# Kernel optimization log

Hardware: AMD Instinct MI355X
Metric: run time of the kernel (lower is better)

Reference implementation:

```python
import jax, jax.numpy as jnp
import numpy as np

V = 50257   # vocab
P = 2048    # max positions
D = 768     # hidden
H = 12      # heads
F = 3072    # 4*D ffn
NL = 12     # layers
L = 2048    # seq len
EPS = 1e-5


def setup_inputs() -> dict:
    key = jax.random.key(0)
    ks = jax.random.split(key, 12)
    r = lambda k, shp: jax.random.normal(k, shp, jnp.float32) * 0.02
    return dict(
        input_ids=jax.random.randint(ks[0], (1, L), 0, V, dtype=jnp.int32),
        attention_mask=jnp.ones((1, L), jnp.int32),
        wte=r(ks[1], (V, D)),
        wpe=r(ks[2], (P, D)),
        lnf_w=jnp.ones((D,), jnp.float32),
        lnf_b=jnp.zeros((D,), jnp.float32),
        ln1_w=jnp.ones((NL, D), jnp.float32),
        ln1_b=jnp.zeros((NL, D), jnp.float32),
        qw=r(ks[3], (NL, D, D)),
        kw=r(ks[4], (NL, D, D)),
        vw=r(ks[5], (NL, D, D)),
        ow=r(ks[6], (NL, D, D)),
        ob=jnp.zeros((NL, D), jnp.float32),
        ln2_w=jnp.ones((NL, D), jnp.float32),
        ln2_b=jnp.zeros((NL, D), jnp.float32),
        fcw=r(ks[7], (NL, D, F)),
        fcb=jnp.zeros((NL, F), jnp.float32),
        pw=r(ks[8], (NL, F, D)),
        pb=jnp.zeros((NL, D), jnp.float32),
    )


def _ln(x, w, b):
    mu = jnp.mean(x, -1, keepdims=True)
    var = jnp.mean((x - mu) ** 2, -1, keepdims=True)
    return (x - mu) * jax.lax.rsqrt(var + EPS) * w + b


def reference(input_ids, attention_mask, wte, wpe, lnf_w, lnf_b,
              ln1_w, ln1_b, qw, kw, vw, ow, ob, ln2_w, ln2_b,
              fcw, fcb, pw, pb):
    ids = input_ids.reshape(-1, input_ids.shape[-1])          # [1, L]
    pos = jnp.cumsum(attention_mask, -1) - 1
    pos = jnp.where(attention_mask == 0, 1, pos)
    h = (wte[ids] + wpe[pos])[0]                               # [L, D]

    key_valid = attention_mask[0] > 0                          # actual_length mask
    mask = jnp.tril(jnp.ones((L, L), bool)) & key_valid[None, :]  # causal+pad
    dh = D // H

    def layer(h, p):
        l1w, l1b, Wq, Wk, Wv, Wo, bo, l2w, l2b, Wf, bf, Wp, bp = p
        x = _ln(h, l1w, l1b)
        q = (x @ Wq).reshape(L, H, dh)
        k = (x @ Wk).reshape(L, H, dh)
        v = (x @ Wv).reshape(L, H, dh)
        # GPT-Neo attention: NO 1/sqrt(dh) scaling
        scores = jnp.einsum('qhd,khd->hqk', q, k)
        scores = jnp.where(mask[None], scores, jnp.float32(-1e9))
        attn = jax.nn.softmax(scores, axis=-1)
        ctx = jnp.einsum('hqk,khd->qhd', attn, v).reshape(L, D)
        h = h + ctx @ Wo + bo
        y = _ln(h, l2w, l2b)
        h = h + jax.nn.gelu(y @ Wf + bf, approximate=True) @ Wp + bp
        return h, None

    h, _ = jax.lax.scan(layer, h, (ln1_w, ln1_b, qw, kw, vw, ow, ob,
                                   ln2_w, ln2_b, fcw, fcb, pw, pb))
    return _ln(h[None, :, :], lnf_w, lnf_b)                    # [1, L, D]
```

## Files before the change

kernel.cpp:

```cpp
#include <hip/hip_runtime.h>
#include <hip/hip_bf16.h>
#include <math.h>
#include <stdint.h>

#define L 2048
#define D 768
#define H 12
#define DH 64
#define F 3072
#define NL 12
#define QKVN 2304

typedef __attribute__((ext_vector_type(8))) short bf16x8;
typedef __attribute__((ext_vector_type(4))) float f32x4;

__device__ __forceinline__ ushort f2bf(float x) {
    union { float f; uint32_t u; } c; c.f = x;
    uint32_t r = c.u + 0x7FFFu + ((c.u >> 16) & 1u);
    return (ushort)(r >> 16);
}

__device__ __forceinline__ uint32_t cvt_pk_bf16(float lo, float hi) {
    uint32_t r;
    asm("v_cvt_pk_bf16_f32 %0, %1, %2" : "=v"(r) : "v"(lo), "v"(hi));
    return r;
}

__device__ __forceinline__ bf16x8 ldfrag(const ushort* p) {
    ushort4 lo = *(const ushort4*)(p);
    ushort4 hi = *(const ushort4*)(p + 16);
    bf16x8 f;
    f[0] = (short)lo.x; f[1] = (short)lo.y; f[2] = (short)lo.z; f[3] = (short)lo.w;
    f[4] = (short)hi.x; f[5] = (short)hi.y; f[6] = (short)hi.z; f[7] = (short)hi.w;
    return f;
}

__device__ __forceinline__ float gelu_tanh(float x) {
    float c = 0.7978845608028654f;
    float inner = c * (x + 0.044715f * x * x * x);
    return 0.5f * x * (1.0f + tanhf(inner));
}

__global__ void pos_kernel(const int* __restrict__ mask, int* __restrict__ pos) {
    __shared__ int sm[L];
    for (int i = threadIdx.x; i < L; i += blockDim.x) sm[i] = mask[i];
    __syncthreads();
    int t = blockIdx.x * blockDim.x + threadIdx.x;
    if (t < L) {
        int s = 0;
        for (int j = 0; j <= t; ++j) s += sm[j];
        int p = s - 1;
        if (sm[t] == 0) p = 1;
        pos[t] = p;
    }
}

__global__ void maskb_kernel(const int* __restrict__ mask, float* __restrict__ mb) {
    int i = blockIdx.x * blockDim.x + threadIdx.x;
    if (i < L) mb[i] = mask[i] ? 0.f : -1e9f;
}

__global__ __launch_bounds__(256) void embed_kernel(const int* __restrict__ ids,
                                                    const int* __restrict__ pos,
                                                    const float* __restrict__ wte,
                                                    const float* __restrict__ wpe,
                                                    float* __restrict__ h) {
    int t = blockIdx.x;
    int id = ids[t];
    int p = pos[t];
    const float* we = wte + (size_t)id * D;
    const float* wp = wpe + (size_t)p * D;
    float* hr = h + (size_t)t * D;
#pragma unroll
    for (int i = 0; i < 3; ++i) {
        int d = threadIdx.x + i * 256;
        hr[d] = we[d] + wp[d];
    }
}

template <bool OUTBF>
__global__ __launch_bounds__(256) void ln_kernel(const float* __restrict__ in,
                                                 const float* __restrict__ w,
                                                 const float* __restrict__ b,
                                                 float* __restrict__ outF,
                                                 ushort* __restrict__ outB) {
    __shared__ float red[2][4];
    int row = blockIdx.x;
    const float* x = in + (size_t)row * D;
    int t = threadIdx.x;
    float v0 = x[t], v1 = x[t + 256], v2 = x[t + 512];
    float s = v0 + v1 + v2;
    float ss = v0 * v0 + v1 * v1 + v2 * v2;
#pragma unroll
    for (int o = 32; o; o >>= 1) {
        s += __shfl_xor(s, o);
        ss += __shfl_xor(ss, o);
    }
    int wave = t >> 6;
    if ((t & 63) == 0) { red[0][wave] = s; red[1][wave] = ss; }
    __syncthreads();
    s = red[0][0] + red[0][1] + red[0][2] + red[0][3];
    ss = red[1][0] + red[1][1] + red[1][2] + red[1][3];
    float mean = s * (1.f / D);
    float var = ss * (1.f / D) - mean * mean;
    float rstd = rsqrtf(var + 1e-5f);
#pragma unroll
    for (int i = 0; i < 3; ++i) {
        int d = t + i * 256;
        float vv = (i == 0) ? v0 : (i == 1) ? v1 : v2;
        float y = (vv - mean) * rstd * w[d] + b[d];
        if (OUTBF) outB[(size_t)row * D + d] = f2bf(y);
        else       outF[(size_t)row * D + d] = y;
    }
}

__global__ __launch_bounds__(256) void tcast_f32(const float* __restrict__ in,
                                                 ushort* __restrict__ out,
                                                 int K, int N,
                                                 size_t inStride, size_t outStride) {
    in += blockIdx.z * inStride;
    out += blockIdx.z * outStride;
    __shared__ float tile[64][65];
    int k0 = blockIdx.y * 64, n0 = blockIdx.x * 64;
    int t = threadIdx.x;
    int cl = t & 63, rg = t >> 6;
#pragma unroll
    for (int i = 0; i < 16; ++i) {
        int r = rg + 4 * i;
        tile[r][cl] = in[(size_t)(k0 + r) * N + n0 + cl];
    }
    __syncthreads();
#pragma unroll
    for (int i = 0; i < 16; ++i) {
        int r = rg + 4 * i;
        out[(size_t)(n0 + r) * K + k0 + cl] = f2bf(tile[cl][r]);
    }
}

template <int ACT, bool OUTBF, bool VSPLIT>
__global__ __launch_bounds__(256) void gemm_bf16(const ushort* __restrict__ A,
                                                 const ushort* __restrict__ Bt,
                                                 const float* __restrict__ bias,
                                                 const float* __restrict__ resid,
                                                 float* __restrict__ outF,
                                                 ushort* __restrict__ outB,
                                                 ushort* __restrict__ vTout,
                                                 int M, int N, int K) {
    __shared__ __align__(16) char lds[32768];
    const int tid = threadIdx.x;
    const int lane = tid & 63, w = tid >> 6;
    const int wr = w >> 1, wc = w & 1;
    const int bm = blockIdx.y * 128, bn = blockIdx.x * 128;
    const int l15 = lane & 15, l4 = lane >> 4;
    const int srow = tid >> 2, c = tid & 3;
    const int blo = (c & 1) * 32 + (c >> 1) * 8;

    const int sxor = (srow & 3) << 4;
    const int wo0 = srow * 64 + (blo ^ sxor);
    const int wo1 = srow * 64 + ((blo + 16) ^ sxor);
    const int rxor = (l4 * 16) ^ ((l15 & 3) << 4);
    const int aBase = (wr * 64 + l15) * 64 + rxor;
    const int bBase = (wc * 64 + l15) * 64 + rxor;

    f32x4 acc[4][4];
#pragma unroll
    for (int m = 0; m < 4; ++m)
#pragma unroll
        for (int n = 0; n < 4; ++n)
            acc[m][n] = (f32x4){0.f, 0.f, 0.f, 0.f};

    const ushort* Ag = A + (size_t)(bm + srow) * K + c * 8;
    const ushort* Ag2 = Ag + (size_t)64 * K;
    const ushort* Bg = Bt + (size_t)(bn + srow) * K + c * 8;
    const ushort* Bg2 = Bg + (size_t)64 * K;

    uint4 a0 = *(const uint4*)(Ag);
    uint4 a1 = *(const uint4*)(Ag2);
    uint4 b0 = *(const uint4*)(Bg);
    uint4 b1 = *(const uint4*)(Bg2);

    for (int k0 = 0; k0 < K; k0 += 32) {
        char* Ab = lds + ((k0 >> 5) & 1) * 16384;
        char* Bb = Ab + 8192;
        uint2 t0, t1;
        t0.x = a0.x; t0.y = a0.y; t1.x = a0.z; t1.y = a0.w;
        *(uint2*)(Ab + wo0) = t0;
        *(uint2*)(Ab + wo1) = t1;
        t0.x = a1.x; t0.y = a1.y; t1.x = a1.z; t1.y = a1.w;
        *(uint2*)(Ab + wo0 + 4096) = t0;
        *(uint2*)(Ab + wo1 + 4096) = t1;
        t0.x = b0.x; t0.y = b0.y; t1.x = b0.z; t1.y = b0.w;
        *(uint2*)(Bb + wo0) = t0;
        *(uint2*)(Bb + wo1) = t1;
        t0.x = b1.x; t0.y = b1.y; t1.x = b1.z; t1.y = b1.w;
        *(uint2*)(Bb + wo0 + 4096) = t0;
        *(uint2*)(Bb + wo1 + 4096) = t1;
        __syncthreads();
        if (k0 + 32 < K) {
            a0 = *(const uint4*)(Ag + k0 + 32);
            a1 = *(const uint4*)(Ag2 + k0 + 32);
            b0 = *(const uint4*)(Bg + k0 + 32);
            b1 = *(const uint4*)(Bg2 + k0 + 32);
        }
        bf16x8 af[4], bfv[4];
#pragma unroll
        for (int m = 0; m < 4; ++m)
            af[m] = *(const bf16x8*)(Ab + aBase + m * 1024);
#pragma unroll
        for (int n = 0; n < 4; ++n)
            bfv[n] = *(const bf16x8*)(Bb + bBase + n * 1024);
#pragma unroll
        for (int m = 0; m < 4; ++m)
#pragma unroll
            for (int n = 0; n < 4; ++n)
                acc[m][n] = __builtin_amdgcn_mfma_f32_16x16x32_bf16(af[m], bfv[n], acc[m][n], 0, 0, 0);
    }

#pragma unroll
    for (int m = 0; m < 4; ++m)
#pragma unroll
        for (int n = 0; n < 4; ++n) {
            int col = bn + wc * 64 + n * 16 + l15;
            int row0 = bm + wr * 64 + m * 16 + l4 * 4;
            if (VSPLIT && col >= 2 * D) {
                ushort4 pk;
                pk.x = f2bf(acc[m][n][0]);
                pk.y = f2bf(acc[m][n][1]);
                pk.z = f2bf(acc[m][n][2]);
                pk.w = f2bf(acc[m][n][3]);
                *(ushort4*)(vTout + (size_t)(col - 2 * D) * L + row0) = pk;
            } else {
#pragma unroll
                for (int r = 0; r < 4; ++r) {
                    int row = row0 + r;
                    float v = acc[m][n][r];
                    if (bias) v += bias[col];
                    if (ACT == 1) v = gelu_tanh(v);
                    if (resid) v += resid[(size_t)row * N + col];
                    if (OUTBF) outB[(size_t)row * N + col] = f2bf(v);
                    else       outF[(size_t)row * N + col] = v;
                }
            }
        }
}

__global__ __launch_bounds__(256) void gemm64_bf16(const ushort* __restrict__ A,
                                                   const ushort* __restrict__ Bt,
                                                   const float* __restrict__ bias,
                                                   float* __restrict__ h,
                                                   int M, int N, int K) {
    __shared__ __align__(16) char lds[32768];
    const int tid = threadIdx.x;
    const int lane = tid & 63, w = tid >> 6;
    const int wr = w >> 1, wc = w & 1;
    const int bm = blockIdx.y * 64, bn = blockIdx.x * 64;
    const int l15 = lane & 15, l4 = lane >> 4;
    const int srow = tid >> 2, q = tid & 3;
    const int swz = (srow & 7) << 4;
    const int rb = srow * 128;
    int offlo[2], offhi[2];
#pragma unroll
    for (int i = 0; i < 2; ++i) {
        int g = 2 * q + i;
        int cc = g & 3, hf = g >> 2;
        int blo = (cc & 1) * 32 + ((cc >> 1) & 1) * 8 + hf * 64;
        offlo[i] = rb + ((blo & 0x70) ^ swz) + (blo & 15);
        int bhi = blo + 16;
        offhi[i] = rb + ((bhi & 0x70) ^ swz) + (bhi & 15);
    }
    const int fxor = (l15 & 7) << 4;

    f32x4 acc[2][2];
#pragma unroll
    for (int m = 0; m < 2; ++m)
#pragma unroll
        for (int n = 0; n < 2; ++n)
            acc[m][n] = (f32x4){0.f, 0.f, 0.f, 0.f};

    const ushort* Ag = A + (size_t)(bm + srow) * K + q * 16;
    const ushort* Bg = Bt + (size_t)(bn + srow) * K + q * 16;

    uint4 a0 = *(const uint4*)(Ag);
    uint4 a1 = *(const uint4*)(Ag + 8);
    uint4 b0 = *(const uint4*)(Bg);
    uint4 b1 = *(const uint4*)(Bg + 8);

    for (int k0 = 0; k0 < K; k0 += 64) {
        char* Ab = lds + ((k0 >> 6) & 1) * 16384;
        char* Bb = Ab + 8192;
        uint2 t0, t1;
        t0.x = a0.x; t0.y = a0.y; t1.x = a0.z; t1.y = a0.w;
        *(uint2*)(Ab + offlo[0]) = t0;
        *(uint2*)(Ab + offhi[0]) = t1;
        t0.x = a1.x; t0.y = a1.y; t1.x = a1.z; t1.y = a1.w;
        *(uint2*)(Ab + offlo[1]) = t0;
        *(uint2*)(Ab + offhi[1]) = t1;
        t0.x = b0.x; t0.y = b0.y; t1.x = b0.z; t1.y = b0.w;
        *(uint2*)(Bb + offlo[0]) = t0;
        *(uint2*)(Bb + offhi[0]) = t1;
        t0.x = b1.x; t0.y = b1.y; t1.x = b1.z; t1.y = b1.w;
        *(uint2*)(Bb + offlo[1]) = t0;
        *(uint2*)(Bb + offhi[1]) = t1;
        __syncthreads();
        if (k0 + 64 < K) {
            a0 = *(const uint4*)(Ag + k0 + 64);
            a1 = *(const uint4*)(Ag + k0 + 72);
            b0 = *(const uint4*)(Bg + k0 + 64);
            b1 = *(const uint4*)(Bg + k0 + 72);
        }
        bf16x8 af[2][2], bfv[2][2];
#pragma unroll
        for (int m = 0; m < 2; ++m)
#pragma unroll
            for (int ks = 0; ks < 2; ++ks)
                af[m][ks] = *(const bf16x8*)(Ab + (wr * 32 + m * 16 + l15) * 128 +
                                             ((ks * 64 + l4 * 16) ^ fxor));
#pragma unroll
        for (int n = 0; n < 2; ++n)
#pragma unroll
            for (int ks = 0; ks < 2; ++ks)
                bfv[n][ks] = *(const bf16x8*)(Bb + (wc * 32 + n * 16 + l15) * 128 +
                                              ((ks * 64 + l4 * 16) ^ fxor));
#pragma unroll
        for (int m = 0; m < 2; ++m)
#pragma unroll
            for (int n = 0; n < 2; ++n)
#pragma unroll
                for (int ks = 0; ks < 2; ++ks)
                    acc[m][n] = __builtin_amdgcn_mfma_f32_16x16x32_bf16(
                        af[m][ks], bfv[n][ks], acc[m][n], 0, 0, 0);
    }

#pragma unroll
    for (int m = 0; m < 2; ++m)
#pragma unroll
        for (int n = 0; n < 2; ++n) {
            int col = bn + wc * 32 + n * 16 + l15;
#pragma unroll
            for (int r = 0; r < 4; ++r) {
                int row = bm + wr * 32 + m * 16 + l4 * 4 + r;
                float v = acc[m][n][r] + bias[col] + h[(size_t)row * N + col];
                h[(size_t)row * N + col] = v;
            }
        }
}

__global__ __launch_bounds__(128) void attn_kernel(const ushort* __restrict__ qkv,
                                                   const ushort* __restrict__ vT,
                                                   const float* __restrict__ maskb,
                                                   ushort* __restrict__ ctx) {
    __shared__ __align__(16) char Kl[2][8192];
    __shared__ __align__(16) char Vl[2][8192];
    __shared__ float Ml[2][64];
    const int hh = blockIdx.y;
    const int q0 = ((int)gridDim.x - 1 - (int)blockIdx.x) * 32;
    const int tid = threadIdx.x;
    const int lane = tid & 63, w = tid >> 6;
    const int l15 = lane & 15, l4 = lane >> 4;
    const int qg = q0 + w * 16 + l15;
    const int qmin = q0 + w * 16;

    bf16x8 qf[2];
#pragma unroll
    for (int ks = 0; ks < 2; ++ks)
        qf[ks] = ldfrag(qkv + (size_t)qg * QKVN + hh * 64 + ks * 32 + l4 * 4);

    f32x4 o[4];
#pragma unroll
    for (int i = 0; i < 4; ++i) o[i] = (f32x4){0.f, 0.f, 0.f, 0.f};
    float mrun = -1e30f, lrun = 0.f;

    const int srow = tid >> 1, hf = tid & 1;
    const int swz = (srow & 7) << 4;
    const int rb = srow * 128;
    int offlo[4], offhi[4];
#pragma unroll
    for (int cc = 0; cc < 4; ++cc) {
        int blo = (cc & 1) * 32 + ((cc >> 1) & 1) * 8 + hf * 64;
        offlo[cc] = rb + ((blo & 0x70) ^ swz) + (blo & 15);
        int bhi = blo + 16;
        offhi[cc] = rb + ((bhi & 0x70) ^ swz) + (bhi & 15);
    }
    const int fxor = (l15 & 7) << 4;

    const ushort* Ksrc = qkv + (size_t)srow * QKVN + D + hh * 64 + hf * 32;
    const ushort* Vsrc = vT + (size_t)(hh * 64 + srow) * L + hf * 32;

    uint4 kx[4], vx[4];
    float mv = 0.f;
    const int nt = q0 / 64 + 1;

#pragma unroll
    for (int cc = 0; cc < 4; ++cc) {
        kx[cc] = *(const uint4*)(Ksrc + cc * 8);
        vx[cc] = *(const uint4*)(Vsrc + cc * 8);
    }
    if (tid < 64) mv = maskb[tid];

    for (int it = 0; it < nt; ++it) {
        const int kv0 = it * 64;
        const int b = it & 1;
        {
            char* Kb = Kl[b];
            char* Vb = Vl[b];
            uint2 t0, t1;
#pragma unroll
            for (int cc = 0; cc < 4; ++cc) {
                t0.x = kx[cc].x; t0.y = kx[cc].y; t1.x = kx[cc].z; t1.y = kx[cc].w;
                *(uint2*)(Kb + offlo[cc]) = t0;
                *(uint2*)(Kb + offhi[cc]) = t1;
                t0.x = vx[cc].x; t0.y = vx[cc].y; t1.x = vx[cc].z; t1.y = vx[cc].w;
                *(uint2*)(Vb + offlo[cc]) = t0;
                *(uint2*)(Vb + offhi[cc]) = t1;
            }
            if (tid < 64) Ml[b][tid] = mv;
        }
        __syncthreads();
        if (it + 1 < nt) {
            const size_t koff = (size_t)(kv0 + 64) * QKVN;
#pragma unroll
            for (int cc = 0; cc < 4; ++cc) {
                kx[cc] = *(const uint4*)(Ksrc + koff + cc * 8);
                vx[cc] = *(const uint4*)(Vsrc + kv0 + 64 + cc * 8);
            }
            if (tid < 64) mv = maskb[kv0 + 64 + tid];
        }

        const char* Kb = Kl[b];
        const char* Vb = Vl[b];

        f32x4 st[4];
#pragma unroll
        for (int m = 0; m < 4; ++m) st[m] = (f32x4){0.f, 0.f, 0.f, 0.f};
#pragma unroll
        for (int m = 0; m < 4; ++m)
#pragma unroll
            for (int ks = 0; ks < 2; ++ks) {
                bf16x8 kf = *(const bf16x8*)(Kb + (m * 16 + l15) * 128 +
                                             ((ks * 64 + l4 * 16) ^ fxor));
                st[m] = __builtin_amdgcn_mfma_f32_16x16x32_bf16(kf, qf[ks], st[m], 0, 0, 0);
            }

        float p[4][4];
        float tmax = -1e30f;
        const bool full = (kv0 + 63 <= qmin);
        if (full) {
#pragma unroll
            for (int m = 0; m < 4; ++m)
#pragma unroll
                for (int r = 0; r < 4; ++r) {
                    int kl = m * 16 + l4 * 4 + r;
                    float s = st[m][r] + Ml[b][kl];
                    p[m][r] = s;
                    tmax = fmaxf(tmax, s);
                }
        } else {
#pragma unroll
            for (int m = 0; m < 4; ++m)
#pragma unroll
                for (int r = 0; r < 4; ++r) {
                    int kl = m * 16 + l4 * 4 + r;
                    float s = st[m][r] + Ml[b][kl];
                    if (kv0 + kl > qg) s = -1e30f;
                    p[m][r] = s;
                    tmax = fmaxf(tmax, s);
                }
        }
        tmax = fmaxf(tmax, __shfl_xor(tmax, 16));
        tmax = fmaxf(tmax, __shfl_xor(tmax, 32));
        const bool noresc = __all(tmax <= mrun);
        float mnew = noresc ? mrun : fmaxf(mrun, tmax);
        float scale = noresc ? 1.f : __expf(mrun - mnew);
        float ts = 0.f;
#pragma unroll
        for (int m = 0; m < 4; ++m)
#pragma unroll
            for (int r = 0; r < 4; ++r) {
                float e = __expf(p[m][r] - mnew);
                p[m][r] = e;
                ts += e;
            }
        ts += __shfl_xor(ts, 16);
        ts += __shfl_xor(ts, 32);
        lrun = lrun * scale + ts;
        mrun = mnew;

        bf16x8 pf[2];
#pragma unroll
        for (int g = 0; g < 2; ++g) {
            union { bf16x8 v; uint32_t d[4]; } pu;
            pu.d[0] = cvt_pk_bf16(p[2 * g][0], p[2 * g][1]);
            pu.d[1] = cvt_pk_bf16(p[2 * g][2], p[2 * g][3]);
            pu.d[2] = cvt_pk_bf16(p[2 * g + 1][0], p[2 * g + 1][1]);
            pu.d[3] = cvt_pk_bf16(p[2 * g + 1][2], p[2 * g + 1][3]);
            pf[g] = pu.v;
        }
        if (!noresc) {
#pragma unroll
            for (int i = 0; i < 4; ++i) {
                o[i][0] *= scale; o[i][1] *= scale; o[i][2] *= scale; o[i][3] *= scale;
            }
        }
#pragma unroll
        for (int dhb = 0; dhb < 4; ++dhb)
#pragma unroll
            for (int g = 0; g < 2; ++g) {
                bf16x8 vf = *(const bf16x8*)(Vb + (dhb * 16 + l15) * 128 +
                                             ((g * 64 + l4 * 16) ^ fxor));
                o[dhb] = __builtin_amdgcn_mfma_f32_16x16x32_bf16(vf, pf[g], o[dhb], 0, 0, 0);
            }
    }

    float rinv = 1.0f / lrun;
#pragma unroll
    for (int dhb = 0; dhb < 4; ++dhb) {
        ushort4 pk;
        pk.x = f2bf(o[dhb][0] * rinv);
        pk.y = f2bf(o[dhb][1] * rinv);
        pk.z = f2bf(o[dhb][2] * rinv);
        pk.w = f2bf(o[dhb][3] * rinv);
        *(ushort4*)(ctx + (size_t)qg * D + hh * 64 + dhb * 16 + l4 * 4) = pk;
    }
}

extern "C" void kernel_launch(void* const* d_in, const int* in_sizes, int n_in,
                              void* d_out, int out_size, void* d_ws, size_t ws_size,
                              hipStream_t stream) {
    const int* ids = (const int*)d_in[0];
    const int* amask = (const int*)d_in[1];
    const float* wte = (const float*)d_in[2];
    const float* wpe = (const float*)d_in[3];
    const float* lnf_w = (const float*)d_in[4];
    const float* lnf_b = (const float*)d_in[5];
    const float* ln1_w = (const float*)d_in[6];
    const float* ln1_b = (const float*)d_in[7];
    const float* qw = (const float*)d_in[8];
    const float* kw = (const float*)d_in[9];
    const float* vw = (const float*)d_in[10];
    const float* ow = (const float*)d_in[11];
    const float* ob = (const float*)d_in[12];
    const float* ln2_w = (const float*)d_in[13];
    const float* ln2_b = (const float*)d_in[14];
    const float* fcw = (const float*)d_in[15];
    const float* fcb = (const float*)d_in[16];
    const float* pw = (const float*)d_in[17];
    const float* pb = (const float*)d_in[18];

    char* p = (char*)d_ws;
    auto take = [&](size_t bytes) -> char* {
        char* r = p;
        p += (bytes + 4095) & ~(size_t)4095;
        return r;
    };
    ushort* wqkvT = (ushort*)take((size_t)NL * QKVN * D * 2);
    ushort* woT   = (ushort*)take((size_t)NL * D * D * 2);
    ushort* fcwT  = (ushort*)take((size_t)NL * F * D * 2);
    ushort* pwT   = (ushort*)take((size_t)NL * D * F * 2);
    float*  h     = (float*)take((size_t)L * D * 4);
    ushort* xb    = (ushort*)take((size_t)L * D * 2);
    ushort* qkvb  = (ushort*)take((size_t)L * QKVN * 2);
    ushort* vTb   = (ushort*)take((size_t)D * L * 2);
    ushort* ctxb  = (ushort*)take((size_t)L * D * 2);
    ushort* f1b   = (ushort*)take((size_t)L * F * 2);
    float*  mb    = (float*)take(L * 4);
    int*    pos   = (int*)take(L * 4);

    pos_kernel<<<8, 256, 0, stream>>>(amask, pos);
    maskb_kernel<<<8, 256, 0, stream>>>(amask, mb);
    embed_kernel<<<L, 256, 0, stream>>>(ids, pos, wte, wpe, h);

    tcast_f32<<<dim3(12, 12, NL), 256, 0, stream>>>(qw, wqkvT, D, D,
                                                    (size_t)D * D, (size_t)QKVN * D);
    tcast_f32<<<dim3(12, 12, NL), 256, 0, stream>>>(kw, wqkvT + (size_t)D * D, D, D,
                                                    (size_t)D * D, (size_t)QKVN * D);
    tcast_f32<<<dim3(12, 12, NL), 256, 0, stream>>>(vw, wqkvT + (size_t)2 * D * D, D, D,
                                                    (size_t)D * D, (size_t)QKVN * D);
    tcast_f32<<<dim3(12, 12, NL), 256, 0, stream>>>(ow, woT, D, D,
                                                    (size_t)D * D, (size_t)D * D);
    tcast_f32<<<dim3(48, 12, NL), 256, 0, stream>>>(fcw, fcwT, D, F,
                                                    (size_t)D * F, (size_t)F * D);
    tcast_f32<<<dim3(12, 48, NL), 256, 0, stream>>>(pw, pwT, F, D,
                                                    (size_t)F * D, (size_t)D * F);

    ln_kernel<true><<<L, 256, 0, stream>>>(h, ln1_w, ln1_b, nullptr, xb);

    for (int l = 0; l < NL; ++l) {
        gemm_bf16<0, true, true><<<dim3(QKVN / 128, L / 128), 256, 0, stream>>>(
            xb, wqkvT + (size_t)l * QKVN * D, nullptr, nullptr, nullptr, qkvb,
            vTb, L, QKVN, D);
        attn_kernel<<<dim3(L / 32, H), 128, 0, stream>>>(qkvb, vTb, mb, ctxb);
        gemm64_bf16<<<dim3(D / 64, L / 64), 256, 0, stream>>>(
            ctxb, woT + (size_t)l * D * D, ob + l * D, h, L, D, D);
        ln_kernel<true><<<L, 256, 0, stream>>>(h, ln2_w + l * D, ln2_b + l * D,
                                               nullptr, xb);
        gemm_bf16<1, true, false><<<dim3(F / 128, L / 128), 256, 0, stream>>>(
            xb, fcwT + (size_t)l * F * D, fcb + l * F, nullptr, nullptr, f1b,
            nullptr, L, F, D);
        gemm64_bf16<<<dim3(D / 64, L / 64), 256, 0, stream>>>(
            f1b, pwT + (size_t)l * D * F, pb + l * D, h, L, D, F);
        if (l < NL - 1) {
            ln_kernel<true><<<L, 256, 0, stream>>>(h, ln1_w + (l + 1) * D,
                                                   ln1_b + (l + 1) * D, nullptr, xb);
        } else {
            ln_kernel<false><<<L, 256, 0, stream>>>(h, lnf_w, lnf_b,
                                                    (float*)d_out, nullptr);
        }
    }
}
```

Baseline: 2.084 ms.

## Swizzle GEMM workgroups across XCDs and widen attention blocks to 64 queries

Adds an XCD-aware remapping of workgroup IDs in both GEMM kernels, so that blocks landing on the same XCD cover contiguous output tiles and share its L2. The attention kernel now uses 256 threads (4 waves) per block covering 64 queries instead of 128 threads covering 32. Each K/V tile loaded into LDS is therefore reused by twice as many waves, and the per-thread staging work drops to two 16-byte loads each for K and V. The risks are fewer blocks for the causal load balance, and that the swizzle assumes the grid size divides evenly by 8.

```diff
diff --git a/kernel.cpp b/kernel.cpp
--- a/kernel.cpp
+++ b/kernel.cpp
@@ -39,6 +39,11 @@
     float c = 0.7978845608028654f;
     float inner = c * (x + 0.044715f * x * x * x);
     return 0.5f * x * (1.0f + tanhf(inner));
+}
+
+__device__ __forceinline__ int xcd_swz(int id, int nwg) {
+    int cpx = nwg >> 3;
+    return (id & 7) * cpx + (id >> 3);
 }
 
 __global__ void pos_kernel(const int* __restrict__ mask, int* __restrict__ pos) {
@@ -150,7 +155,9 @@
     const int tid = threadIdx.x;
     const int lane = tid & 63, w = tid >> 6;
     const int wr = w >> 1, wc = w & 1;
-    const int bm = blockIdx.y * 128, bn = blockIdx.x * 128;
+    const int nwg = gridDim.x * gridDim.y;
+    const int sid = xcd_swz(blockIdx.y * gridDim.x + blockIdx.x, nwg);
+    const int bm = (sid / gridDim.x) * 128, bn = (sid % gridDim.x) * 128;
     const int l15 = lane & 15, l4 = lane >> 4;
     const int srow = tid >> 2, c = tid & 3;
     const int blo = (c & 1) * 32 + (c >> 1) * 8;
@@ -253,7 +260,9 @@
     const int tid = threadIdx.x;
     const int lane = tid & 63, w = tid >> 6;
     const int wr = w >> 1, wc = w & 1;
-    const int bm = blockIdx.y * 64, bn = blockIdx.x * 64;
+    const int nwg = gridDim.x * gridDim.y;
+    const int sid = xcd_swz(blockIdx.y * gridDim.x + blockIdx.x, nwg);
+    const int bm = (sid / gridDim.x) * 64, bn = (sid % gridDim.x) * 64;
     const int l15 = lane & 15, l4 = lane >> 4;
     const int srow = tid >> 2, q = tid & 3;
     const int swz = (srow & 7) << 4;
@@ -345,7 +354,7 @@
         }
 }
 
-__global__ __launch_bounds__(128) void attn_kernel(const ushort* __restrict__ qkv,
+__global__ __launch_bounds__(256) void attn_kernel(const ushort* __restrict__ qkv,
                                                    const ushort* __restrict__ vT,
                                                    const float* __restrict__ maskb,
                                                    ushort* __restrict__ ctx) {
@@ -353,7 +362,7 @@
     __shared__ __align__(16) char Vl[2][8192];
     __shared__ float Ml[2][64];
     const int hh = blockIdx.y;
-    const int q0 = ((int)gridDim.x - 1 - (int)blockIdx.x) * 32;
+    const int q0 = ((int)gridDim.x - 1 - (int)blockIdx.x) * 64;
     const int tid = threadIdx.x;
     const int lane = tid & 63, w = tid >> 6;
     const int l15 = lane & 15, l4 = lane >> 4;
@@ -370,32 +379,31 @@
     for (int i = 0; i < 4; ++i) o[i] = (f32x4){0.f, 0.f, 0.f, 0.f};
     float mrun = -1e30f, lrun = 0.f;
 
-    const int srow = tid >> 1, hf = tid & 1;
+    const int srow = tid >> 2, c = tid & 3;
+    const int blo = (c & 1) * 32 + (c >> 1) * 8;
     const int swz = (srow & 7) << 4;
     const int rb = srow * 128;
-    int offlo[4], offhi[4];
-#pragma unroll
-    for (int cc = 0; cc < 4; ++cc) {
-        int blo = (cc & 1) * 32 + ((cc >> 1) & 1) * 8 + hf * 64;
-        offlo[cc] = rb + ((blo & 0x70) ^ swz) + (blo & 15);
-        int bhi = blo + 16;
-        offhi[cc] = rb + ((bhi & 0x70) ^ swz) + (bhi & 15);
-    }
+    const int lo4 = blo & 15;
+    const int s0 = rb + (((blo)      & 0x70) ^ swz) + lo4;
+    const int s1 = rb + (((blo + 16) & 0x70) ^ swz) + lo4;
+    const int s2 = rb + (((blo + 64) & 0x70) ^ swz) + lo4;
+    const int s3 = rb + (((blo + 80) & 0x70) ^ swz) + lo4;
     const int fxor = (l15 & 7) << 4;
 
-    const ushort* Ksrc = qkv + (size_t)srow * QKVN + D + hh * 64 + hf * 32;
-    const ushort* Vsrc = vT + (size_t)(hh * 64 + srow) * L + hf * 32;
-
-    uint4 kx[4], vx[4];
+    const ushort* Ksrc = qkv + (size_t)srow * QKVN + D + hh * 64 + c * 8;
+    const ushort* Vsrc = vT + (size_t)(hh * 64 + srow) * L + c * 8;
+
+    uint4 ka, kb, va, vb;
     float mv = 0.f;
     const int nt = q0 / 64 + 1;
 
-#pragma unroll
-    for (int cc = 0; cc < 4; ++cc) {
-        kx[cc] = *(const uint4*)(Ksrc + cc * 8);
-        vx[cc] = *(const uint4*)(Vsrc + cc * 8);
-    }
-    if (tid < 64) mv = maskb[tid];
+    {
+        ka = *(const uint4*)(Ksrc);
+        kb = *(const uint4*)(Ksrc + 32);
+        va = *(const uint4*)(Vsrc);
+        vb = *(const uint4*)(Vsrc + 32);
+        if (tid < 64) mv = maskb[tid];
+    }
 
     for (int it = 0; it < nt; ++it) {
         const int kv0 = it * 64;
@@ -404,25 +412,27 @@
             char* Kb = Kl[b];
             char* Vb = Vl[b];
             uint2 t0, t1;
-#pragma unroll
-            for (int cc = 0; cc < 4; ++cc) {
-                t0.x = kx[cc].x; t0.y = kx[cc].y; t1.x = kx[cc].z; t1.y = kx[cc].w;
-                *(uint2*)(Kb + offlo[cc]) = t0;
-                *(uint2*)(Kb + offhi[cc]) = t1;
-                t0.x = vx[cc].x; t0.y = vx[cc].y; t1.x = vx[cc].z; t1.y = vx[cc].w;
-                *(uint2*)(Vb + offlo[cc]) = t0;
-                *(uint2*)(Vb + offhi[cc]) = t1;
-            }
+            t0.x = ka.x; t0.y = ka.y; t1.x = ka.z; t1.y = ka.w;
+            *(uint2*)(Kb + s0) = t0;
+            *(uint2*)(Kb + s1) = t1;
+            t0.x = kb.x; t0.y = kb.y; t1.x = kb.z; t1.y = kb.w;
+            *(uint2*)(Kb + s2) = t0;
+            *(uint2*)(Kb + s3) = t1;
+            t0.x = va.x; t0.y = va.y; t1.x = va.z; t1.y = va.w;
+            *(uint2*)(Vb + s0) = t0;
+            *(uint2*)(Vb + s1) = t1;
+            t0.x = vb.x; t0.y = vb.y; t1.x = vb.z; t1.y = vb.w;
+            *(uint2*)(Vb + s2) = t0;
+            *(uint2*)(Vb + s3) = t1;
             if (tid < 64) Ml[b][tid] = mv;
         }
         __syncthreads();
         if (it + 1 < nt) {
             const size_t koff = (size_t)(kv0 + 64) * QKVN;
-#pragma unroll
-            for (int cc = 0; cc < 4; ++cc) {
-                kx[cc] = *(const uint4*)(Ksrc + koff + cc * 8);
-                vx[cc] = *(const uint4*)(Vsrc + kv0 + 64 + cc * 8);
-            }
+            ka = *(const uint4*)(Ksrc + koff);
+            kb = *(const uint4*)(Ksrc + koff + 32);
+            va = *(const uint4*)(Vsrc + kv0 + 64);
+            vb = *(const uint4*)(Vsrc + kv0 + 96);
             if (tid < 64) mv = maskb[kv0 + 64 + tid];
         }
 
@@ -588,7 +598,7 @@
         gemm_bf16<0, true, true><<<dim3(QKVN / 128, L / 128), 256, 0, stream>>>(
             xb, wqkvT + (size_t)l * QKVN * D, nullptr, nullptr, nullptr, qkvb,
             vTb, L, QKVN, D);
-        attn_kernel<<<dim3(L / 32, H), 128, 0, stream>>>(qkvb, vTb, mb, ctxb);
+        attn_kernel<<<dim3(L / 64, H), 256, 0, stream>>>(qkvb, vTb, mb, ctxb);
         gemm64_bf16<<<dim3(D / 64, L / 64), 256, 0, stream>>>(
             ctxb, woT + (size_t)l * D * D, ob + l * D, h, L, D, D);
         ln_kernel<true><<<L, 256, 0, stream>>>(h, ln2_w + l * D, ln2_b + l * D,
```

New measurement: 2.013 ms. -3.4%, faster.
